# Kernel optimization log

Measured on AMD Instinct MI355X. Metric: run time of the kernel, lower is better.

## Reference

```python
import jax, jax.numpy as jnp
import numpy as np

C_IN, C_OUT, K, H, W = 16, 16, 3, 1024, 1024
PAD = 1  # 'same' padding for 3x3 stride-1


def setup_inputs() -> dict:
    key = jax.random.key(0)
    kx, kw, kb = jax.random.split(key, 3)
    x = jax.random.normal(kx, (1, C_IN, H, W), dtype=jnp.float32)
    weight = jax.random.normal(kw, (C_OUT, C_IN, K, K), dtype=jnp.float32) * 0.05
    bias = jax.random.normal(kb, (C_OUT,), dtype=jnp.float32) * 0.05
    return {"x": x, "weight": weight, "bias": bias}


def reference(x, weight, bias):
    # Original module: im2col (unfold) + matmul + reshape + bias add.
    # Mathematically identical to a dense 2D convolution (cross-correlation),
    # expressed here as the fused implicit-GEMM conv primitive.
    out = jax.lax.conv_general_dilated(
        x, weight,
        window_strides=(1, 1),
        padding=((PAD, PAD), (PAD, PAD)),
        dimension_numbers=("NCHW", "OIHW", "NCHW"),
    )  # [1, C_OUT, H, W]
    # out_unf.view(*output_shape) drops the batch dim (batch must be 1)
    return out[0] + bias[:, None, None]
```

## Files before the change

kernel.cpp:

```cpp
#include <hip/hip_runtime.h>


#define HH 1024
#define WW 1024
#define CIN 16
#define HWP (HH * WW)
#define TW 64
#define TH 8
#define LROWS 10
#define LCOLS 66
#define NPIX (LROWS * LCOLS)

typedef short v8s __attribute__((ext_vector_type(8)));
typedef float v4f __attribute__((ext_vector_type(4)));
typedef unsigned int u32;

__device__ __forceinline__ u32 cvt_pk_bf16(float lo, float hi) {
    u32 r;
    asm("v_cvt_pk_bf16_f32 %0, %1, %2" : "=v"(r) : "v"(lo), "v"(hi));
    return r;
}

__device__ __forceinline__ int swz(int c) { return c ^ ((c >> 3) & 7); }

__global__ __launch_bounds__(64, 2)
void conv3x3_wave(const float* __restrict__ x,
                  const float* __restrict__ wgt,
                  const float* __restrict__ bias,
                  float* __restrict__ out) {
    __shared__ __align__(16) unsigned short sm[NPIX * 16];

    const int lane = threadIdx.x;
    const int m = lane & 15;
    const int q = lane >> 4;
    const int w0 = blockIdx.x * TW;
    const int h0 = blockIdx.y * TH;

    v8s a[5];
    #pragma unroll
    for (int g5 = 0; g5 < 5; ++g5) {
        const int t = 4 * g5 + q;
        union { u32 u[4]; v8s v; } wv;
        if (t < 18) {
            const int base = m * 144 + (t & 1) * 72 + (t >> 1);
            #pragma unroll
            for (int jj = 0; jj < 4; ++jj) {
                const float lo = wgt[base + 18 * jj];
                const float hi = wgt[base + 18 * jj + 9];
                wv.u[jj] = cvt_pk_bf16(lo, hi);
            }
        } else {
            wv.u[0] = wv.u[1] = wv.u[2] = wv.u[3] = 0u;
        }
        a[g5] = wv.v;
    }
    float bl[4];
    #pragma unroll
    for (int i = 0; i < 4; ++i) bl[i] = bias[q * 4 + i];

    int Kbase[5];
    #pragma unroll
    for (int g5 = 0; g5 < 5; ++g5) {
        int t = 4 * g5 + q;
        int tt = t > 17 ? 17 : t;
        int khkw = tt >> 1;
        int kh = khkw / 3;
        int kw = khkw - 3 * kh;
        Kbase[g5] = (kh * LCOLS + m + kw) * 2 + (tt & 1);
    }

    auto load_body = [&](int s0, int NR, float4* f4) {
        const int rr = lane >> 4;
        if (rr < NR) {
            const int gh = h0 - 1 + s0 + rr;
            const int j = lane & 15;
            if ((unsigned)gh < (unsigned)HH) {
                const float4* src = (const float4*)(x + (size_t)gh * WW + w0) + j;
                #pragma unroll
                for (int c = 0; c < CIN; ++c)
                    f4[c] = src[(size_t)c * (HWP / 4)];
            } else {
                #pragma unroll
                for (int c = 0; c < CIN; ++c)
                    f4[c] = make_float4(0.f, 0.f, 0.f, 0.f);
            }
        }
    };
    auto load_halo = [&](int s0, int NR, int lane0, float* f) {
        const int h = lane - lane0;
        if ((unsigned)h < (unsigned)(2 * NR)) {
            const int gh = h0 - 1 + s0 + (h >> 1);
            const int gw = (h & 1) ? (w0 + TW) : (w0 - 1);
            if ((unsigned)gh < (unsigned)HH && (unsigned)gw < (unsigned)WW) {
                const float* src = x + (size_t)gh * WW + gw;
                #pragma unroll
                for (int c = 0; c < CIN; ++c) f[c] = src[(size_t)c * HWP];
            } else {
                #pragma unroll
                for (int c = 0; c < CIN; ++c) f[c] = 0.f;
            }
        }
    };
    auto write_body = [&](int s0, int NR, const float4* f4) {
        const int rr = lane >> 4;
        if (rr < NR) {
            const int slot = s0 + rr;
            const int j = lane & 15;
            const int pbase = slot * LCOLS + 1 + 4 * j;
            #pragma unroll
            for (int k = 0; k < 4; ++k) {
                u32 pk[8];
                #pragma unroll
                for (int i = 0; i < 8; ++i) {
                    const float lo = ((const float*)&f4[2 * i])[k];
                    const float hi = ((const float*)&f4[2 * i + 1])[k];
                    pk[i] = cvt_pk_bf16(lo, hi);
                }
                #pragma unroll
                for (int half = 0; half < 2; ++half) {
                    const int cc = 2 * pbase + 2 * k + half;
                    *(uint4*)(sm + swz(cc) * 8) = *(uint4*)&pk[half * 4];
                }
            }
        }
    };
    auto write_halo = [&](int s0, int NR, int lane0, const float* f) {
        const int h = lane - lane0;
        if ((unsigned)h < (unsigned)(2 * NR)) {
            const int slot = s0 + (h >> 1);
            const int p = slot * LCOLS + ((h & 1) ? 65 : 0);
            u32 pk[8];
            #pragma unroll
            for (int i = 0; i < 8; ++i)
                pk[i] = cvt_pk_bf16(f[2 * i], f[2 * i + 1]);
            #pragma unroll
            for (int half = 0; half < 2; ++half) {
                const int cc = 2 * p + half;
                *(uint4*)(sm + swz(cc) * 8) = *(uint4*)&pk[half * 4];
            }
        }
    };

    auto compute4 = [&](int r0) {
        #pragma unroll
        for (int rr = 0; rr < 4; ++rr) {
            const int r = r0 + rr;
            #pragma unroll
            for (int g16 = 0; g16 < 4; ++g16) {
                v4f acc = {0.f, 0.f, 0.f, 0.f};
                #pragma unroll
                for (int g5 = 0; g5 < 5; ++g5) {
                    const int c = r * (LCOLS * 2) + g16 * 32 + Kbase[g5];
                    v8s b = *(const v8s*)(sm + swz(c) * 8);
                    acc = __builtin_amdgcn_mfma_f32_16x16x32_bf16(a[g5], b, acc, 0, 0, 0);
                }
                float* op = out + (size_t)(h0 + r) * WW + (w0 + g16 * 16 + m);
                #pragma unroll
                for (int i = 0; i < 4; ++i)
                    op[(size_t)(q * 4 + i) * HWP] = acc[i] + bl[i];
            }
        }
    };

    float4 fA[CIN];
    float4 fB[CIN];
    float hA[CIN], hB[CIN], hC[CIN];

    load_body(0, 4, fA);  load_halo(0, 4, 0, hA);
    load_body(4, 4, fB);  load_halo(4, 4, 0, hB);
    write_body(0, 4, fA); write_halo(0, 4, 0, hA);
    load_body(8, 2, fA);  load_halo(8, 2, 32, hC);
    write_body(4, 4, fB); write_halo(4, 4, 0, hB);
    write_body(8, 2, fA); write_halo(8, 2, 32, hC);
    compute4(0);
    compute4(4);
}

extern "C" void kernel_launch(void* const* d_in, const int* in_sizes, int n_in,
                              void* d_out, int out_size, void* d_ws, size_t ws_size,
                              hipStream_t stream) {
    const float* x = (const float*)d_in[0];
    const float* w = (const float*)d_in[1];
    const float* b = (const float*)d_in[2];
    float* out = (float*)d_out;
    dim3 grid(WW / TW, HH / TH);
    conv3x3_wave<<<grid, dim3(64), 0, stream>>>(x, w, b, out);
}
```

Measured before the change: 139.8 us.

## Use 4-wave blocks with a 16-row LDS ring buffer and pipelined row loads

```diff
diff --git a/kernel.cpp b/kernel.cpp
--- a/kernel.cpp
+++ b/kernel.cpp
@@ -6,10 +6,10 @@
 #define CIN 16
 #define HWP (HH * WW)
 #define TW 64
-#define TH 8
-#define LROWS 10
+#define CH 16
 #define LCOLS 66
-#define NPIX (LROWS * LCOLS)
+#define RS 16
+#define CPR (LCOLS * 2)
 
 typedef short v8s __attribute__((ext_vector_type(8)));
 typedef float v4f __attribute__((ext_vector_type(4)));
@@ -23,18 +23,28 @@
 
 __device__ __forceinline__ int swz(int c) { return c ^ ((c >> 3) & 7); }
 
-__global__ __launch_bounds__(64, 2)
-void conv3x3_wave(const float* __restrict__ x,
+__device__ __forceinline__ void wave_barrier() {
+    __builtin_amdgcn_sched_barrier(0);
+    asm volatile("s_waitcnt lgkmcnt(0)" ::: "memory");
+    __builtin_amdgcn_sched_barrier(0);
+    __builtin_amdgcn_s_barrier();
+    __builtin_amdgcn_sched_barrier(0);
+}
+
+__global__ __launch_bounds__(256, 4)
+void conv3x3_ring(const float* __restrict__ x,
                   const float* __restrict__ wgt,
                   const float* __restrict__ bias,
                   float* __restrict__ out) {
-    __shared__ __align__(16) unsigned short sm[NPIX * 16];
-
-    const int lane = threadIdx.x;
+    __shared__ __align__(16) unsigned short sm[RS * LCOLS * 16];
+
+    const int tid = threadIdx.x;
+    const int lane = tid & 63;
+    const int wave = tid >> 6;
     const int m = lane & 15;
     const int q = lane >> 4;
     const int w0 = blockIdx.x * TW;
-    const int h0 = blockIdx.y * TH;
+    const int h0 = blockIdx.y * CH;
 
     v8s a[5];
     #pragma unroll
@@ -58,7 +68,7 @@
     #pragma unroll
     for (int i = 0; i < 4; ++i) bl[i] = bias[q * 4 + i];
 
-    int Kbase[5];
+    int Koff[5], kh5[5];
     #pragma unroll
     for (int g5 = 0; g5 < 5; ++g5) {
         int t = 4 * g5 + q;
@@ -66,114 +76,123 @@
         int khkw = tt >> 1;
         int kh = khkw / 3;
         int kw = khkw - 3 * kh;
-        Kbase[g5] = (kh * LCOLS + m + kw) * 2 + (tt & 1);
+        kh5[g5] = kh;
+        Koff[g5] = (m + kw) * 2 + (tt & 1);
     }
 
-    auto load_body = [&](int s0, int NR, float4* f4) {
-        const int rr = lane >> 4;
-        if (rr < NR) {
-            const int gh = h0 - 1 + s0 + rr;
-            const int j = lane & 15;
+    auto loadB = [&](int G, float* f) {
+        const int nr = (G == 4) ? 2 : 4;
+        const int rr = tid >> 6;
+        if (rr < nr) {
+            const int gh = h0 - 1 + 4 * G + rr;
+            const int gw = w0 + (tid & 63);
             if ((unsigned)gh < (unsigned)HH) {
-                const float4* src = (const float4*)(x + (size_t)gh * WW + w0) + j;
-                #pragma unroll
-                for (int c = 0; c < CIN; ++c)
-                    f4[c] = src[(size_t)c * (HWP / 4)];
+                const float* p = x + (size_t)gh * WW + gw;
+                #pragma unroll
+                for (int c = 0; c < CIN; ++c) f[c] = p[(size_t)c * HWP];
             } else {
                 #pragma unroll
-                for (int c = 0; c < CIN; ++c)
-                    f4[c] = make_float4(0.f, 0.f, 0.f, 0.f);
-            }
-        }
-    };
-    auto load_halo = [&](int s0, int NR, int lane0, float* f) {
-        const int h = lane - lane0;
-        if ((unsigned)h < (unsigned)(2 * NR)) {
-            const int gh = h0 - 1 + s0 + (h >> 1);
-            const int gw = (h & 1) ? (w0 + TW) : (w0 - 1);
-            if ((unsigned)gh < (unsigned)HH && (unsigned)gw < (unsigned)WW) {
-                const float* src = x + (size_t)gh * WW + gw;
-                #pragma unroll
-                for (int c = 0; c < CIN; ++c) f[c] = src[(size_t)c * HWP];
-            } else {
-                #pragma unroll
                 for (int c = 0; c < CIN; ++c) f[c] = 0.f;
             }
         }
     };
-    auto write_body = [&](int s0, int NR, const float4* f4) {
-        const int rr = lane >> 4;
-        if (rr < NR) {
-            const int slot = s0 + rr;
-            const int j = lane & 15;
-            const int pbase = slot * LCOLS + 1 + 4 * j;
-            #pragma unroll
-            for (int k = 0; k < 4; ++k) {
-                u32 pk[8];
-                #pragma unroll
-                for (int i = 0; i < 8; ++i) {
-                    const float lo = ((const float*)&f4[2 * i])[k];
-                    const float hi = ((const float*)&f4[2 * i + 1])[k];
-                    pk[i] = cvt_pk_bf16(lo, hi);
-                }
-                #pragma unroll
-                for (int half = 0; half < 2; ++half) {
-                    const int cc = 2 * pbase + 2 * k + half;
-                    *(uint4*)(sm + swz(cc) * 8) = *(uint4*)&pk[half * 4];
-                }
-            }
-        }
-    };
-    auto write_halo = [&](int s0, int NR, int lane0, const float* f) {
-        const int h = lane - lane0;
-        if ((unsigned)h < (unsigned)(2 * NR)) {
-            const int slot = s0 + (h >> 1);
-            const int p = slot * LCOLS + ((h & 1) ? 65 : 0);
+    auto writeB = [&](int G, const float* f) {
+        const int nr = (G == 4) ? 2 : 4;
+        const int rr = tid >> 6;
+        if (rr < nr) {
+            const int slot = (4 * G + rr) & (RS - 1);
+            const int p = slot * LCOLS + (tid & 63) + 1;
             u32 pk[8];
             #pragma unroll
             for (int i = 0; i < 8; ++i)
                 pk[i] = cvt_pk_bf16(f[2 * i], f[2 * i + 1]);
-            #pragma unroll
-            for (int half = 0; half < 2; ++half) {
-                const int cc = 2 * p + half;
-                *(uint4*)(sm + swz(cc) * 8) = *(uint4*)&pk[half * 4];
-            }
-        }
-    };
-
-    auto compute4 = [&](int r0) {
+            *(uint4*)(sm + swz(2 * p) * 8)     = *(uint4*)&pk[0];
+            *(uint4*)(sm + swz(2 * p + 1) * 8) = *(uint4*)&pk[4];
+        }
+    };
+    auto loadH = [&](int G, float* f) {
+        const int nh = (G == 4) ? 4 : 8;
+        if (tid < nh) {
+            const int gh = h0 - 1 + 4 * G + (tid >> 1);
+            const int gw = (tid & 1) ? (w0 + TW) : (w0 - 1);
+            if ((unsigned)gh < (unsigned)HH && (unsigned)gw < (unsigned)WW) {
+                const float* p = x + (size_t)gh * WW + gw;
+                #pragma unroll
+                for (int c = 0; c < CIN; ++c) f[c] = p[(size_t)c * HWP];
+            } else {
+                #pragma unroll
+                for (int c = 0; c < CIN; ++c) f[c] = 0.f;
+            }
+        }
+    };
+    auto writeH = [&](int G, const float* f) {
+        const int nh = (G == 4) ? 4 : 8;
+        if (tid < nh) {
+            const int slot = (4 * G + (tid >> 1)) & (RS - 1);
+            const int p = slot * LCOLS + ((tid & 1) ? 65 : 0);
+            u32 pk[8];
+            #pragma unroll
+            for (int i = 0; i < 8; ++i)
+                pk[i] = cvt_pk_bf16(f[2 * i], f[2 * i + 1]);
+            *(uint4*)(sm + swz(2 * p) * 8)     = *(uint4*)&pk[0];
+            *(uint4*)(sm + swz(2 * p + 1) * 8) = *(uint4*)&pk[4];
+        }
+    };
+
+    auto compute = [&](int g) {
+        const int R = h0 + 4 * g + wave;
         #pragma unroll
-        for (int rr = 0; rr < 4; ++rr) {
-            const int r = r0 + rr;
-            #pragma unroll
-            for (int g16 = 0; g16 < 4; ++g16) {
-                v4f acc = {0.f, 0.f, 0.f, 0.f};
-                #pragma unroll
-                for (int g5 = 0; g5 < 5; ++g5) {
-                    const int c = r * (LCOLS * 2) + g16 * 32 + Kbase[g5];
-                    v8s b = *(const v8s*)(sm + swz(c) * 8);
-                    acc = __builtin_amdgcn_mfma_f32_16x16x32_bf16(a[g5], b, acc, 0, 0, 0);
-                }
-                float* op = out + (size_t)(h0 + r) * WW + (w0 + g16 * 16 + m);
-                #pragma unroll
-                for (int i = 0; i < 4; ++i)
-                    op[(size_t)(q * 4 + i) * HWP] = acc[i] + bl[i];
-            }
-        }
-    };
-
-    float4 fA[CIN];
-    float4 fB[CIN];
-    float hA[CIN], hB[CIN], hC[CIN];
-
-    load_body(0, 4, fA);  load_halo(0, 4, 0, hA);
-    load_body(4, 4, fB);  load_halo(4, 4, 0, hB);
-    write_body(0, 4, fA); write_halo(0, 4, 0, hA);
-    load_body(8, 2, fA);  load_halo(8, 2, 32, hC);
-    write_body(4, 4, fB); write_halo(4, 4, 0, hB);
-    write_body(8, 2, fA); write_halo(8, 2, 32, hC);
-    compute4(0);
-    compute4(4);
+        for (int cg = 0; cg < 4; ++cg) {
+            v4f acc = {0.f, 0.f, 0.f, 0.f};
+            #pragma unroll
+            for (int g5 = 0; g5 < 5; ++g5) {
+                const int slot = (4 * g + wave + kh5[g5]) & (RS - 1);
+                const int c = slot * CPR + cg * 32 + Koff[g5];
+                v8s b = *(const v8s*)(sm + swz(c) * 8);
+                acc = __builtin_amdgcn_mfma_f32_16x16x32_bf16(a[g5], b, acc, 0, 0, 0);
+            }
+            float* op = out + (size_t)R * WW + (w0 + cg * 16 + m);
+            #pragma unroll
+            for (int i = 0; i < 4; ++i)
+                op[(size_t)(q * 4 + i) * HWP] = acc[i] + bl[i];
+        }
+        __builtin_amdgcn_sched_barrier(0);
+    };
+
+    float f0[CIN], f1[CIN], fh[CIN];
+    loadB(0, f0);
+    loadB(1, f1);
+    loadH(0, fh);
+    writeB(0, f0);
+    writeH(0, fh);
+    loadH(1, fh);
+    writeB(1, f1);
+    writeH(1, fh);
+    loadB(2, f0);
+    loadH(2, fh);
+    __builtin_amdgcn_sched_barrier(0);
+    wave_barrier();
+
+    compute(0);
+    loadB(3, f1);
+    writeB(2, f0);
+    writeH(2, fh);
+    loadH(3, fh);
+    wave_barrier();
+
+    compute(1);
+    loadB(4, f0);
+    writeB(3, f1);
+    writeH(3, fh);
+    loadH(4, fh);
+    wave_barrier();
+
+    compute(2);
+    writeB(4, f0);
+    writeH(4, fh);
+    wave_barrier();
+
+    compute(3);
 }
 
 extern "C" void kernel_launch(void* const* d_in, const int* in_sizes, int n_in,
@@ -183,6 +202,6 @@
     const float* w = (const float*)d_in[1];
     const float* b = (const float*)d_in[2];
     float* out = (float*)d_out;
-    dim3 grid(WW / TW, HH / TH);
-    conv3x3_wave<<<grid, dim3(64), 0, stream>>>(x, w, b, out);
-}
+    dim3 grid(WW / TW, HH / CH);
+    conv3x3_ring<<<grid, dim3(256), 0, stream>>>(x, w, b, out);
+}
```

After: 140.9 us. About the same (+0.8%).

## Restructure conv into 4 independent waves per block with separate halo LDS region

Applied to the files above, without the earlier changes.

```diff
diff --git a/kernel.cpp b/kernel.cpp
--- a/kernel.cpp
+++ b/kernel.cpp
@@ -6,10 +6,10 @@
 #define CIN 16
 #define HWP (HH * WW)
 #define TW 64
-#define TH 8
-#define LROWS 10
-#define LCOLS 66
-#define NPIX (LROWS * LCOLS)
+#define RPW 4
+#define WPB 4
+#define HCB 768
+#define WLDS 6336
 
 typedef short v8s __attribute__((ext_vector_type(8)));
 typedef float v4f __attribute__((ext_vector_type(4)));
@@ -23,18 +23,21 @@
 
 __device__ __forceinline__ int swz(int c) { return c ^ ((c >> 3) & 7); }
 
-__global__ __launch_bounds__(64, 2)
-void conv3x3_wave(const float* __restrict__ x,
-                  const float* __restrict__ wgt,
-                  const float* __restrict__ bias,
-                  float* __restrict__ out) {
-    __shared__ __align__(16) unsigned short sm[NPIX * 16];
+__global__ __launch_bounds__(256, 3)
+void conv3x3_iw(const float* __restrict__ x,
+                const float* __restrict__ wgt,
+                const float* __restrict__ bias,
+                float* __restrict__ out) {
+    __shared__ __align__(16) unsigned short sm[WPB * WLDS];
 
-    const int lane = threadIdx.x;
+    const int tid = threadIdx.x;
+    const int lane = tid & 63;
+    const int wave = tid >> 6;
     const int m = lane & 15;
     const int q = lane >> 4;
     const int w0 = blockIdx.x * TW;
-    const int h0 = blockIdx.y * TH;
+    const int y0 = (blockIdx.y * WPB + wave) * RPW;
+    unsigned short* smw = sm + wave * WLDS;
 
     v8s a[5];
     #pragma unroll
@@ -58,7 +61,7 @@
     #pragma unroll
     for (int i = 0; i < 4; ++i) bl[i] = bias[q * 4 + i];
 
-    int Kbase[5];
+    int mkw[5], hf5[5], kh5[5];
     #pragma unroll
     for (int g5 = 0; g5 < 5; ++g5) {
         int t = 4 * g5 + q;
@@ -66,95 +69,87 @@
         int khkw = tt >> 1;
         int kh = khkw / 3;
         int kw = khkw - 3 * kh;
-        Kbase[g5] = (kh * LCOLS + m + kw) * 2 + (tt & 1);
+        kh5[g5] = kh;
+        mkw[g5] = m + kw;
+        hf5[g5] = tt & 1;
     }
 
-    auto load_body = [&](int s0, int NR, float4* f4) {
-        const int rr = lane >> 4;
-        if (rr < NR) {
-            const int gh = h0 - 1 + s0 + rr;
-            const int j = lane & 15;
+    auto loadS = [&](int s, float* f) {
+        #pragma unroll
+        for (int z = 0; z < 2; ++z) {
+            const int gh = y0 - 1 + 2 * s + z;
             if ((unsigned)gh < (unsigned)HH) {
-                const float4* src = (const float4*)(x + (size_t)gh * WW + w0) + j;
+                const float* p = x + (size_t)gh * WW + (w0 + lane);
                 #pragma unroll
                 for (int c = 0; c < CIN; ++c)
-                    f4[c] = src[(size_t)c * (HWP / 4)];
+                    f[z * 16 + c] = p[(size_t)c * HWP];
             } else {
                 #pragma unroll
                 for (int c = 0; c < CIN; ++c)
-                    f4[c] = make_float4(0.f, 0.f, 0.f, 0.f);
+                    f[z * 16 + c] = 0.f;
             }
         }
     };
-    auto load_halo = [&](int s0, int NR, int lane0, float* f) {
-        const int h = lane - lane0;
-        if ((unsigned)h < (unsigned)(2 * NR)) {
-            const int gh = h0 - 1 + s0 + (h >> 1);
-            const int gw = (h & 1) ? (w0 + TW) : (w0 - 1);
+    auto writeS = [&](int s, const float* f) {
+        #pragma unroll
+        for (int z = 0; z < 2; ++z) {
+            const int slot = 2 * s + z;
+            u32 pk[8];
+            #pragma unroll
+            for (int i = 0; i < 8; ++i)
+                pk[i] = cvt_pk_bf16(f[z * 16 + 2 * i], f[z * 16 + 2 * i + 1]);
+            const int c0 = slot * 128 + lane * 2;
+            *(uint4*)(smw + swz(c0) * 8)     = *(uint4*)&pk[0];
+            *(uint4*)(smw + swz(c0 + 1) * 8) = *(uint4*)&pk[4];
+        }
+    };
+
+    float2 hA, hB;
+    auto haloLoad = [&](int j, float2& fp) {
+        const int p = lane + 64 * j;
+        if (p < 96) {
+            const int hp = p >> 3, pc = p & 7;
+            const int slot = hp >> 1, side = hp & 1;
+            const int gh = y0 - 1 + slot;
+            const int gw = side ? (w0 + TW) : (w0 - 1);
             if ((unsigned)gh < (unsigned)HH && (unsigned)gw < (unsigned)WW) {
-                const float* src = x + (size_t)gh * WW + gw;
-                #pragma unroll
-                for (int c = 0; c < CIN; ++c) f[c] = src[(size_t)c * HWP];
+                const float* p2 = x + (size_t)gh * WW + gw;
+                fp.x = p2[(size_t)(2 * pc) * HWP];
+                fp.y = p2[(size_t)(2 * pc + 1) * HWP];
             } else {
-                #pragma unroll
-                for (int c = 0; c < CIN; ++c) f[c] = 0.f;
+                fp.x = 0.f; fp.y = 0.f;
             }
         }
     };
-    auto write_body = [&](int s0, int NR, const float4* f4) {
-        const int rr = lane >> 4;
-        if (rr < NR) {
-            const int slot = s0 + rr;
-            const int j = lane & 15;
-            const int pbase = slot * LCOLS + 1 + 4 * j;
-            #pragma unroll
-            for (int k = 0; k < 4; ++k) {
-                u32 pk[8];
-                #pragma unroll
-                for (int i = 0; i < 8; ++i) {
-                    const float lo = ((const float*)&f4[2 * i])[k];
-                    const float hi = ((const float*)&f4[2 * i + 1])[k];
-                    pk[i] = cvt_pk_bf16(lo, hi);
-                }
-                #pragma unroll
-                for (int half = 0; half < 2; ++half) {
-                    const int cc = 2 * pbase + 2 * k + half;
-                    *(uint4*)(sm + swz(cc) * 8) = *(uint4*)&pk[half * 4];
-                }
-            }
-        }
-    };
-    auto write_halo = [&](int s0, int NR, int lane0, const float* f) {
-        const int h = lane - lane0;
-        if ((unsigned)h < (unsigned)(2 * NR)) {
-            const int slot = s0 + (h >> 1);
-            const int p = slot * LCOLS + ((h & 1) ? 65 : 0);
-            u32 pk[8];
-            #pragma unroll
-            for (int i = 0; i < 8; ++i)
-                pk[i] = cvt_pk_bf16(f[2 * i], f[2 * i + 1]);
-            #pragma unroll
-            for (int half = 0; half < 2; ++half) {
-                const int cc = 2 * p + half;
-                *(uint4*)(sm + swz(cc) * 8) = *(uint4*)&pk[half * 4];
-            }
+    auto haloWrite = [&](int j, float2 fp) {
+        const int p = lane + 64 * j;
+        if (p < 96) {
+            const int hp = p >> 3, pc = p & 7;
+            const u32 pk = cvt_pk_bf16(fp.x, fp.y);
+            const int ch = HCB + hp * 2 + (pc >> 2);
+            *(u32*)(smw + ch * 8 + (pc & 3) * 2) = pk;
         }
     };
 
-    auto compute4 = [&](int r0) {
+    auto computeP = [&](int k) {
         #pragma unroll
-        for (int rr = 0; rr < 4; ++rr) {
-            const int r = r0 + rr;
+        for (int rr = 0; rr < 2; ++rr) {
+            const int ib = 2 * k + rr;
+            const int R = y0 + ib;
             #pragma unroll
             for (int g16 = 0; g16 < 4; ++g16) {
                 v4f acc = {0.f, 0.f, 0.f, 0.f};
                 #pragma unroll
                 for (int g5 = 0; g5 < 5; ++g5) {
-                    const int c = r * (LCOLS * 2) + g16 * 32 + Kbase[g5];
-                    v8s b = *(const v8s*)(sm + swz(c) * 8);
+                    const int slot = ib + kh5[g5];
+                    const int col = g16 * 16 + mkw[g5] - 1;
+                    const int cb = swz(slot * 128 + (col & 63) * 2 + hf5[g5]);
+                    const int chl = HCB + slot * 4 + ((col == 64) ? 2 : 0) + hf5[g5];
+                    const int c = ((unsigned)col < 64u) ? cb : chl;
+                    v8s b = *(const v8s*)(smw + c * 8);
                     acc = __builtin_amdgcn_mfma_f32_16x16x32_bf16(a[g5], b, acc, 0, 0, 0);
                 }
-                float* op = out + (size_t)(h0 + r) * WW + (w0 + g16 * 16 + m);
+                float* op = out + (size_t)R * WW + (w0 + g16 * 16 + m);
                 #pragma unroll
                 for (int i = 0; i < 4; ++i)
                     op[(size_t)(q * 4 + i) * HWP] = acc[i] + bl[i];
@@ -162,18 +157,19 @@
         }
     };
 
-    float4 fA[CIN];
-    float4 fB[CIN];
-    float hA[CIN], hB[CIN], hC[CIN];
-
-    load_body(0, 4, fA);  load_halo(0, 4, 0, hA);
-    load_body(4, 4, fB);  load_halo(4, 4, 0, hB);
-    write_body(0, 4, fA); write_halo(0, 4, 0, hA);
-    load_body(8, 2, fA);  load_halo(8, 2, 32, hC);
-    write_body(4, 4, fB); write_halo(4, 4, 0, hB);
-    write_body(8, 2, fA); write_halo(8, 2, 32, hC);
-    compute4(0);
-    compute4(4);
+    float A[32], B[32];
+    loadS(0, A);
+    loadS(1, B);
+    haloLoad(0, hA);
+    haloLoad(1, hB);
+    haloWrite(0, hA);
+    haloWrite(1, hB);
+    writeS(0, A);
+    loadS(2, A);
+    writeS(1, B);
+    computeP(0);
+    writeS(2, A);
+    computeP(1);
 }
 
 extern "C" void kernel_launch(void* const* d_in, const int* in_sizes, int n_in,
@@ -183,6 +179,6 @@
     const float* w = (const float*)d_in[1];
     const float* b = (const float*)d_in[2];
     float* out = (float*)d_out;
-    dim3 grid(WW / TW, HH / TH);
-    conv3x3_wave<<<grid, dim3(64), 0, stream>>>(x, w, b, out);
+    dim3 grid(WW / TW, HH / (RPW * WPB));
+    conv3x3_iw<<<grid, dim3(256), 0, stream>>>(x, w, b, out);
 }
```

Measured after the change: 147.6 us. 1.06x slower.
